# Optimization experiments

Hardware: AMD Instinct MI355X
Metric: run time of the kernel (lower is better)

## Reference

```python
import jax, jax.numpy as jnp
import numpy as np

_POW2_VALUES = np.array([-1.0, -0.5, -0.25, -0.125, -0.0625, -0.03125, -0.015625, -0.0078125,
                         0.0, 0.0078125, 0.015625, 0.03125, 0.0625, 0.125, 0.25, 0.5, 1.0],
                        dtype=np.float32)


def setup_inputs() -> dict:
    key = jax.random.key(0)
    B, C, W, H = 16, 256, 56, 56  # ResNet-like activation map
    x = jax.random.normal(key, (B, C, W, H), dtype=jnp.float32)
    pow2_values = jnp.asarray(_POW2_VALUES)  # (K,) codebook, K=17
    return {"x": x, "pow2_values": pow2_values}


def reference(x, pow2_values):
    # For each element of x, find nearest codebook entry (argmin over K) and gather it.
    # |x[..., None] - v| has shape (B, C, W, H, K); argmin reduces the small K axis.
    idxs = jnp.argmin(jnp.abs(x[..., None] - pow2_values), axis=-1)
    return pow2_values[idxs]  # same shape as x
```

## Files before the change

kernel.cpp:

```cpp
#include <hip/hip_runtime.h>
#include <stdint.h>

__device__ __forceinline__ float pow2_quant(float x) {
    uint32_t b    = __float_as_uint(x);
    uint32_t sign = b & 0x80000000u;
    uint32_t a    = b & 0x7FFFFFFFu;
    uint32_t mant = a & 0x007FFFFFu;
    int e = (int)(a >> 23) - 127;

    bool up = sign ? (mant >= 0x00400000u) : (mant > 0x00400000u);
    int e2 = e + (up ? 1 : 0);

    int ec = e2 > 0 ? 0 : (e2 < -7 ? -7 : e2);
    uint32_t magbits = (uint32_t)(127 + ec) << 23;

    bool zero = sign ? (a < 0x3B800000u) : (a <= 0x3B800000u);
    uint32_t res = (zero ? 0u : magbits) | sign;
    return __uint_as_float(res);
}

__global__ void __launch_bounds__(256) pow2quant_kernel(const float* __restrict__ in,
                                                        float* __restrict__ out,
                                                        int n) {
    const int n4 = n >> 2;
    const float4* __restrict__ in4  = (const float4*)in;
    float4* __restrict__ out4 = (float4*)out;

    int stride = gridDim.x * blockDim.x;
    for (int i = blockIdx.x * blockDim.x + threadIdx.x; i < n4; i += stride) {
        float4 v = in4[i];
        float4 r;
        r.x = pow2_quant(v.x);
        r.y = pow2_quant(v.y);
        r.z = pow2_quant(v.z);
        r.w = pow2_quant(v.w);
        out4[i] = r;
    }

    int tail_start = n4 << 2;
    int ti = blockIdx.x * blockDim.x + threadIdx.x;
    if (ti < n - tail_start) {
        out[tail_start + ti] = pow2_quant(in[tail_start + ti]);
    }
}

extern "C" void kernel_launch(void* const* d_in, const int* in_sizes, int n_in,
                              void* d_out, int out_size, void* d_ws, size_t ws_size,
                              hipStream_t stream) {
    const float* x = (const float*)d_in[0];
    float* out = (float*)d_out;
    int n = in_sizes[0];

    int n4 = n >> 2;
    int blocks = (n4 + 255) / 256;
    if (blocks > 2048) blocks = 2048;
    if (blocks < 1) blocks = 1;
    pow2quant_kernel<<<blocks, 256, 0, stream>>>(x, out, n);
}
```

Baseline: 99.51 us.

## Use nontemporal loads/stores with two float4s per thread and no grid cap

Replaces the grid-stride loop with a launch sized to cover half the float4 elements, so each thread loads two float4 values from separated halves before computing and storing. Loads and stores use nontemporal builtins to bypass cache retention for this streaming pass. The 2048-block cap is removed, so many more blocks launch, trading loop overhead for more memory-level parallelism per thread.

```diff
diff --git a/kernel.cpp b/kernel.cpp
--- a/kernel.cpp
+++ b/kernel.cpp
@@ -1,5 +1,7 @@
 #include <hip/hip_runtime.h>
 #include <stdint.h>
+
+typedef float __attribute__((ext_vector_type(4))) f32x4;
 
 __device__ __forceinline__ float pow2_quant(float x) {
     uint32_t b    = __float_as_uint(x);
@@ -19,26 +21,41 @@
     return __uint_as_float(res);
 }
 
+__device__ __forceinline__ f32x4 pow2_quant4(f32x4 v) {
+    f32x4 r;
+    r.x = pow2_quant(v.x);
+    r.y = pow2_quant(v.y);
+    r.z = pow2_quant(v.z);
+    r.w = pow2_quant(v.w);
+    return r;
+}
+
 __global__ void __launch_bounds__(256) pow2quant_kernel(const float* __restrict__ in,
                                                         float* __restrict__ out,
                                                         int n) {
-    const int n4 = n >> 2;
-    const float4* __restrict__ in4  = (const float4*)in;
-    float4* __restrict__ out4 = (float4*)out;
+    const int n4   = n >> 2;
+    const int half = (n4 + 1) >> 1;
+    const f32x4* __restrict__ in4  = (const f32x4*)in;
+    f32x4* __restrict__ out4 = (f32x4*)out;
 
-    int stride = gridDim.x * blockDim.x;
-    for (int i = blockIdx.x * blockDim.x + threadIdx.x; i < n4; i += stride) {
-        float4 v = in4[i];
-        float4 r;
-        r.x = pow2_quant(v.x);
-        r.y = pow2_quant(v.y);
-        r.z = pow2_quant(v.z);
-        r.w = pow2_quant(v.w);
-        out4[i] = r;
+    int i = blockIdx.x * blockDim.x + threadIdx.x;
+    if (i < half) {
+        f32x4 v0 = __builtin_nontemporal_load(in4 + i);
+        const int j = i + half;
+        const bool has2 = (j < n4);
+        f32x4 v1 = {};
+        if (has2) v1 = __builtin_nontemporal_load(in4 + j);
+
+        f32x4 r0 = pow2_quant4(v0);
+        __builtin_nontemporal_store(r0, out4 + i);
+        if (has2) {
+            f32x4 r1 = pow2_quant4(v1);
+            __builtin_nontemporal_store(r1, out4 + j);
+        }
     }
 
-    int tail_start = n4 << 2;
-    int ti = blockIdx.x * blockDim.x + threadIdx.x;
+    const int tail_start = n4 << 2;
+    const int ti = blockIdx.x * blockDim.x + threadIdx.x;
     if (ti < n - tail_start) {
         out[tail_start + ti] = pow2_quant(in[tail_start + ti]);
     }
@@ -49,11 +66,11 @@
                               hipStream_t stream) {
     const float* x = (const float*)d_in[0];
     float* out = (float*)d_out;
-    int n = in_sizes[0];
+    const int n = in_sizes[0];
 
-    int n4 = n >> 2;
-    int blocks = (n4 + 255) / 256;
-    if (blocks > 2048) blocks = 2048;
+    const int n4   = n >> 2;
+    const int half = (n4 + 1) >> 1;
+    int blocks = (half + 255) / 256;
     if (blocks < 1) blocks = 1;
     pow2quant_kernel<<<blocks, 256, 0, stream>>>(x, out, n);
 }
```

Result: slower. 103.1 us (+3.6%).
